# Kernel optimization log

Measured on AMD Instinct MI355X. Metric: run time of the kernel, lower is better.

## Reference

```python
import jax, jax.numpy as jnp
import numpy as np

B, T, D, U = 64, 4096, 256, 64

def setup_inputs() -> dict:
    key = jax.random.key(0)
    k1, k2, k3 = jax.random.split(key, 3)
    inputs = jax.random.normal(k1, (B, T, D), dtype=jnp.float32)
    # glorot_uniform init for W (D,U) and u (U,1); zeros bias
    limW = float(np.sqrt(6.0 / (D + U)))
    W = jax.random.uniform(k2, (D, U), minval=-limW, maxval=limW, dtype=jnp.float32)
    limu = float(np.sqrt(6.0 / (U + 1)))
    u = jax.random.uniform(k3, (U, 1), minval=-limu, maxval=limu, dtype=jnp.float32)
    b = jnp.zeros((U,), dtype=jnp.float32)
    return {"inputs": inputs, "W": W, "b": b, "u": u}

def reference(inputs, W, b, u):
    # score: [B,T,U] = tanh(inputs @ W + b)
    score = jnp.tanh(jnp.einsum('btd,du->btu', inputs, W) + b)
    # logits: [B,T,1]; softmax over time axis (axis=1)
    logits = jnp.einsum('btu,uo->bto', score, u)
    attention_weights = jax.nn.softmax(logits, axis=1)
    # weighted sum over time -> [B,D]
    context = jnp.sum(inputs * attention_weights, axis=1)
    return (context, attention_weights)
```

## Files before the change

kernel.cpp:

```cpp
#include <hip/hip_runtime.h>
#include <math.h>

#define B_ 64
#define T_ 4096
#define D_ 256
#define U_ 64
#define BPB 8
#define RPB (T_ / BPB)
#define NCH (RPB / 64)

typedef float f32x4 __attribute__((ext_vector_type(4)));
typedef short bf16x8 __attribute__((ext_vector_type(8)));

__device__ __forceinline__ unsigned short f2bf_rne(float f) {
    unsigned u = __float_as_uint(f);
    unsigned r = u + 0x7fffu + ((u >> 16) & 1u);
    return (unsigned short)(r >> 16);
}
__device__ __forceinline__ float bfbits2f(unsigned short s) {
    return __uint_as_float(((unsigned)s) << 16);
}

__global__ __launch_bounds__(256) void wprep_kernel(
    const float* __restrict__ W, unsigned short* __restrict__ whi,
    unsigned short* __restrict__ wlo)
{
    int fi = blockIdx.x * 256 + threadIdx.x;
    int j    = fi & 7;
    int lane = (fi >> 3) & 63;
    int tile = fi >> 9;
    int nt = tile & 3, ks = tile >> 2;
    int k = ks * 32 + (lane >> 4) * 8 + j;
    int n = nt * 16 + (lane & 15);
    float w = W[k * U_ + n];
    unsigned short hi = f2bf_rne(w);
    unsigned short lo = f2bf_rne(w - bfbits2f(hi));
    whi[fi] = hi;
    wlo[fi] = lo;
}

__global__ __launch_bounds__(256, 2) void fused_main(
    const float* __restrict__ x, const unsigned short* __restrict__ whi,
    const unsigned short* __restrict__ wlo, const float* __restrict__ bias,
    const float* __restrict__ uvec, float* __restrict__ wts,
    float* __restrict__ Zp, float* __restrict__ Pp)
{
    __shared__ unsigned short Bh[16384];
    __shared__ unsigned short Bl[16384];
    __shared__ float esh[RPB];
    __shared__ float zred[4];

    int tid = threadIdx.x;
    {
        const uint4* sh = (const uint4*)whi;
        const uint4* sl = (const uint4*)wlo;
        uint4* dh = (uint4*)Bh;
        uint4* dl = (uint4*)Bl;
#pragma unroll
        for (int i = 0; i < 8; ++i) {
            dh[tid + i * 256] = sh[tid + i * 256];
            dl[tid + i * 256] = sl[tid + i * 256];
        }
    }
    __syncthreads();

    int lane = tid & 63, wid = tid >> 6;
    int q = lane >> 4, r = lane & 15;
    int b = blockIdx.x / BPB;
    int pb = blockIdx.x % BPB;
    size_t row00 = (size_t)b * T_ + (size_t)pb * RPB;
    const float* xlane = x + (row00 + wid * 16 + r) * D_ + q * 8;
    float* wbase = wts + row00;

    const bf16x8* BhV = (const bf16x8*)Bh;
    const bf16x8* BlV = (const bf16x8*)Bl;

    float zacc = 0.f;

#pragma unroll 1
    for (int c = 0; c < NCH; ++c) {
        const float* xp = xlane + (size_t)c * 64 * D_;
        float4 xb[16];
#pragma unroll
        for (int ks = 0; ks < 8; ++ks) {
            xb[2 * ks]     = *(const float4*)(xp + ks * 32);
            xb[2 * ks + 1] = *(const float4*)(xp + ks * 32 + 4);
        }

        f32x4 acc[4];
#pragma unroll
        for (int nt = 0; nt < 4; ++nt) acc[nt] = (f32x4){0.f, 0.f, 0.f, 0.f};

#pragma unroll
        for (int ks = 0; ks < 8; ++ks) {
            float4 va = xb[2 * ks], vb = xb[2 * ks + 1];
            float f[8] = {va.x, va.y, va.z, va.w, vb.x, vb.y, vb.z, vb.w};
            union { bf16x8 v; unsigned short s[8]; } hi_, lo_;
#pragma unroll
            for (int j = 0; j < 8; ++j) {
                unsigned short a = f2bf_rne(f[j]);
                hi_.s[j] = a;
                lo_.s[j] = f2bf_rne(f[j] - bfbits2f(a));
            }
#pragma unroll
            for (int nt = 0; nt < 4; ++nt) {
                bf16x8 bh = BhV[(ks * 4 + nt) * 64 + lane];
                bf16x8 bl = BlV[(ks * 4 + nt) * 64 + lane];
                acc[nt] = __builtin_amdgcn_mfma_f32_16x16x32_bf16(hi_.v, bh, acc[nt], 0, 0, 0);
                acc[nt] = __builtin_amdgcn_mfma_f32_16x16x32_bf16(hi_.v, bl, acc[nt], 0, 0, 0);
                acc[nt] = __builtin_amdgcn_mfma_f32_16x16x32_bf16(lo_.v, bh, acc[nt], 0, 0, 0);
            }
        }

        float p0 = 0.f, p1 = 0.f, p2 = 0.f, p3 = 0.f;
#pragma unroll
        for (int nt = 0; nt < 4; ++nt) {
            int col = nt * 16 + r;
            float bv = bias[col], uv = uvec[col];
            float s0 = acc[nt][0] + bv, s1 = acc[nt][1] + bv,
                  s2 = acc[nt][2] + bv, s3 = acc[nt][3] + bv;
            p0 = fmaf(1.f - 2.f / (__expf(2.f * s0) + 1.f), uv, p0);
            p1 = fmaf(1.f - 2.f / (__expf(2.f * s1) + 1.f), uv, p1);
            p2 = fmaf(1.f - 2.f / (__expf(2.f * s2) + 1.f), uv, p2);
            p3 = fmaf(1.f - 2.f / (__expf(2.f * s3) + 1.f), uv, p3);
        }
#pragma unroll
        for (int off = 1; off < 16; off <<= 1) {
            p0 += __shfl_xor(p0, off, 64);
            p1 += __shfl_xor(p1, off, 64);
            p2 += __shfl_xor(p2, off, 64);
            p3 += __shfl_xor(p3, off, 64);
        }
        float e0 = __expf(p0), e1 = __expf(p1), e2 = __expf(p2), e3 = __expf(p3);
        if (r == 0) {
            float4 o = {e0, e1, e2, e3};
            int lr = c * 64 + wid * 16 + q * 4;
            *(float4*)(wbase + lr) = o;
            *(float4*)(&esh[lr]) = o;
        }
        zacc += (e0 + e1) + (e2 + e3);
    }

    zacc += __shfl_xor(zacc, 16, 64);
    zacc += __shfl_xor(zacc, 32, 64);
    if (lane == 0) zred[wid] = zacc;
    __syncthreads();
    if (tid == 0) Zp[blockIdx.x] = (zred[0] + zred[1]) + (zred[2] + zred[3]);

    const float* xc = x + row00 * D_ + tid;
    float P0 = 0.f, P1 = 0.f, P2 = 0.f, P3 = 0.f;
#pragma unroll 2
    for (int row = 0; row < RPB; row += 8) {
        float e0 = esh[row + 0], e1 = esh[row + 1], e2 = esh[row + 2], e3 = esh[row + 3];
        float e4 = esh[row + 4], e5 = esh[row + 5], e6 = esh[row + 6], e7 = esh[row + 7];
        float x0 = xc[(size_t)(row + 0) * D_];
        float x1 = xc[(size_t)(row + 1) * D_];
        float x2 = xc[(size_t)(row + 2) * D_];
        float x3 = xc[(size_t)(row + 3) * D_];
        float x4 = xc[(size_t)(row + 4) * D_];
        float x5 = xc[(size_t)(row + 5) * D_];
        float x6 = xc[(size_t)(row + 6) * D_];
        float x7 = xc[(size_t)(row + 7) * D_];
        P0 = fmaf(e0, x0, P0); P1 = fmaf(e1, x1, P1);
        P2 = fmaf(e2, x2, P2); P3 = fmaf(e3, x3, P3);
        P0 = fmaf(e4, x4, P0); P1 = fmaf(e5, x5, P1);
        P2 = fmaf(e6, x6, P2); P3 = fmaf(e7, x7, P3);
    }
    Pp[(size_t)blockIdx.x * D_ + tid] = (P0 + P1) + (P2 + P3);
}

__global__ __launch_bounds__(256) void finalize_kernel(
    float* __restrict__ wts, const float* __restrict__ Zp,
    const float* __restrict__ Pp, float* __restrict__ ctx)
{
    int b = blockIdx.x;
    int tid = threadIdx.x;
    float Z = 0.f;
#pragma unroll
    for (int i = 0; i < BPB; ++i) Z += Zp[b * BPB + i];
    float invZ = 1.f / Z;

    float s = 0.f;
#pragma unroll
    for (int i = 0; i < BPB; ++i) s += Pp[(size_t)(b * BPB + i) * D_ + tid];
    ctx[b * D_ + tid] = s * invZ;

    float4* wp = (float4*)(wts + (size_t)b * T_);
#pragma unroll
    for (int i = 0; i < T_ / 4 / 256; ++i) {
        float4 v = wp[tid + i * 256];
        v.x *= invZ; v.y *= invZ; v.z *= invZ; v.w *= invZ;
        wp[tid + i * 256] = v;
    }
}

extern "C" void kernel_launch(void* const* d_in, const int* in_sizes, int n_in,
                              void* d_out, int out_size, void* d_ws, size_t ws_size,
                              hipStream_t stream) {
    const float* x    = (const float*)d_in[0];
    const float* W    = (const float*)d_in[1];
    const float* bias = (const float*)d_in[2];
    const float* uvec = (const float*)d_in[3];

    float* out = (float*)d_out;
    float* ctx = out;
    float* wts = out + B_ * D_;

    unsigned short* whi = (unsigned short*)d_ws;
    unsigned short* wlo = whi + D_ * U_;
    float* Zp = (float*)(wlo + D_ * U_);
    float* Pp = Zp + B_ * BPB;

    wprep_kernel<<<D_ * U_ / 256, 256, 0, stream>>>(W, whi, wlo);
    fused_main<<<B_ * BPB, 256, 0, stream>>>(x, whi, wlo, bias, uvec, wts, Zp, Pp);
    finalize_kernel<<<B_, 256, 0, stream>>>(wts, Zp, Pp, ctx);
}
```

Before: 454.5 us.

## Split GEMM columns across waves and stage bf16 x in LDS for context

Blocks now cover 64 rows instead of 512, so the grid grows eightfold. Each wave owns one 16-column slice of U and keeps its W hi/lo fragments in registers instead of LDS. The bf16-hi copy of x is stored in LDS, and the weighted-sum pass reads it from there rather than re-reading fp32 x from global memory, removing the second pass over x. The costs are that every wave now reads and splits the same x rows (4x redundant loads and conversion ALU work), context is accumulated from bf16-rounded x, and finalize has more partials to reduce.

```diff
diff --git a/kernel.cpp b/kernel.cpp
--- a/kernel.cpp
+++ b/kernel.cpp
@@ -5,9 +5,10 @@
 #define T_ 4096
 #define D_ 256
 #define U_ 64
-#define BPB 8
-#define RPB (T_ / BPB)
-#define NCH (RPB / 64)
+#define RPB 64
+#define NPB (T_ / RPB)
+#define NSTRIP (RPB / 16)
+#define XPAD 264
 
 typedef float f32x4 __attribute__((ext_vector_type(4)));
 typedef short bf16x8 __attribute__((ext_vector_type(8)));
@@ -39,91 +40,77 @@
     wlo[fi] = lo;
 }
 
-__global__ __launch_bounds__(256, 2) void fused_main(
+__global__ __launch_bounds__(256, 4) void fused_main(
     const float* __restrict__ x, const unsigned short* __restrict__ whi,
     const unsigned short* __restrict__ wlo, const float* __restrict__ bias,
     const float* __restrict__ uvec, float* __restrict__ wts,
     float* __restrict__ Zp, float* __restrict__ Pp)
 {
-    __shared__ unsigned short Bh[16384];
-    __shared__ unsigned short Bl[16384];
+    __shared__ unsigned short Xh[RPB * XPAD];
+    __shared__ float part[RPB][4];
     __shared__ float esh[RPB];
-    __shared__ float zred[4];
 
     int tid = threadIdx.x;
-    {
-        const uint4* sh = (const uint4*)whi;
-        const uint4* sl = (const uint4*)wlo;
-        uint4* dh = (uint4*)Bh;
-        uint4* dl = (uint4*)Bl;
-#pragma unroll
-        for (int i = 0; i < 8; ++i) {
-            dh[tid + i * 256] = sh[tid + i * 256];
-            dl[tid + i * 256] = sl[tid + i * 256];
-        }
-    }
-    __syncthreads();
-
     int lane = tid & 63, wid = tid >> 6;
     int q = lane >> 4, r = lane & 15;
-    int b = blockIdx.x / BPB;
-    int pb = blockIdx.x % BPB;
+
+    bf16x8 Bh[8], Bl[8];
+    {
+        const bf16x8* whiV = (const bf16x8*)whi;
+        const bf16x8* wloV = (const bf16x8*)wlo;
+#pragma unroll
+        for (int ks = 0; ks < 8; ++ks) {
+            Bh[ks] = whiV[(ks * 4 + wid) * 64 + lane];
+            Bl[ks] = wloV[(ks * 4 + wid) * 64 + lane];
+        }
+    }
+
+    int b = blockIdx.x / NPB;
+    int pb = blockIdx.x % NPB;
     size_t row00 = (size_t)b * T_ + (size_t)pb * RPB;
-    const float* xlane = x + (row00 + wid * 16 + r) * D_ + q * 8;
-    float* wbase = wts + row00;
-
-    const bf16x8* BhV = (const bf16x8*)Bh;
-    const bf16x8* BlV = (const bf16x8*)Bl;
-
-    float zacc = 0.f;
+
+    int col = wid * 16 + r;
+    float bv = bias[col], uv = uvec[col];
+
+    const float* xrow = x + (row00 + r) * D_ + q * 8;
 
 #pragma unroll 1
-    for (int c = 0; c < NCH; ++c) {
-        const float* xp = xlane + (size_t)c * 64 * D_;
-        float4 xb[16];
-#pragma unroll
-        for (int ks = 0; ks < 8; ++ks) {
-            xb[2 * ks]     = *(const float4*)(xp + ks * 32);
-            xb[2 * ks + 1] = *(const float4*)(xp + ks * 32 + 4);
-        }
-
-        f32x4 acc[4];
-#pragma unroll
-        for (int nt = 0; nt < 4; ++nt) acc[nt] = (f32x4){0.f, 0.f, 0.f, 0.f};
-
-#pragma unroll
-        for (int ks = 0; ks < 8; ++ks) {
-            float4 va = xb[2 * ks], vb = xb[2 * ks + 1];
-            float f[8] = {va.x, va.y, va.z, va.w, vb.x, vb.y, vb.z, vb.w};
-            union { bf16x8 v; unsigned short s[8]; } hi_, lo_;
-#pragma unroll
-            for (int j = 0; j < 8; ++j) {
-                unsigned short a = f2bf_rne(f[j]);
-                hi_.s[j] = a;
-                lo_.s[j] = f2bf_rne(f[j] - bfbits2f(a));
+    for (int s = 0; s < NSTRIP; ++s) {
+        const float* xp = xrow + (size_t)s * 16 * D_;
+        f32x4 acc = (f32x4){0.f, 0.f, 0.f, 0.f};
+
+#pragma unroll
+        for (int h = 0; h < 2; ++h) {
+            float4 xb[8];
+#pragma unroll
+            for (int k2 = 0; k2 < 4; ++k2) {
+                xb[2 * k2]     = *(const float4*)(xp + (h * 4 + k2) * 32);
+                xb[2 * k2 + 1] = *(const float4*)(xp + (h * 4 + k2) * 32 + 4);
             }
 #pragma unroll
-            for (int nt = 0; nt < 4; ++nt) {
-                bf16x8 bh = BhV[(ks * 4 + nt) * 64 + lane];
-                bf16x8 bl = BlV[(ks * 4 + nt) * 64 + lane];
-                acc[nt] = __builtin_amdgcn_mfma_f32_16x16x32_bf16(hi_.v, bh, acc[nt], 0, 0, 0);
-                acc[nt] = __builtin_amdgcn_mfma_f32_16x16x32_bf16(hi_.v, bl, acc[nt], 0, 0, 0);
-                acc[nt] = __builtin_amdgcn_mfma_f32_16x16x32_bf16(lo_.v, bh, acc[nt], 0, 0, 0);
+            for (int k2 = 0; k2 < 4; ++k2) {
+                int ks = h * 4 + k2;
+                float4 va = xb[2 * k2], vb = xb[2 * k2 + 1];
+                float f[8] = {va.x, va.y, va.z, va.w, vb.x, vb.y, vb.z, vb.w};
+                union { bf16x8 v; unsigned short sh[8]; uint4 u; } hi_, lo_;
+#pragma unroll
+                for (int j = 0; j < 8; ++j) {
+                    unsigned short a = f2bf_rne(f[j]);
+                    hi_.sh[j] = a;
+                    lo_.sh[j] = f2bf_rne(f[j] - bfbits2f(a));
+                }
+                if (wid == 0)
+                    *(uint4*)(&Xh[(s * 16 + r) * XPAD + ks * 32 + q * 8]) = hi_.u;
+                acc = __builtin_amdgcn_mfma_f32_16x16x32_bf16(hi_.v, Bh[ks], acc, 0, 0, 0);
+                acc = __builtin_amdgcn_mfma_f32_16x16x32_bf16(hi_.v, Bl[ks], acc, 0, 0, 0);
+                acc = __builtin_amdgcn_mfma_f32_16x16x32_bf16(lo_.v, Bh[ks], acc, 0, 0, 0);
             }
         }
 
-        float p0 = 0.f, p1 = 0.f, p2 = 0.f, p3 = 0.f;
-#pragma unroll
-        for (int nt = 0; nt < 4; ++nt) {
-            int col = nt * 16 + r;
-            float bv = bias[col], uv = uvec[col];
-            float s0 = acc[nt][0] + bv, s1 = acc[nt][1] + bv,
-                  s2 = acc[nt][2] + bv, s3 = acc[nt][3] + bv;
-            p0 = fmaf(1.f - 2.f / (__expf(2.f * s0) + 1.f), uv, p0);
-            p1 = fmaf(1.f - 2.f / (__expf(2.f * s1) + 1.f), uv, p1);
-            p2 = fmaf(1.f - 2.f / (__expf(2.f * s2) + 1.f), uv, p2);
-            p3 = fmaf(1.f - 2.f / (__expf(2.f * s3) + 1.f), uv, p3);
-        }
+        float p0 = fmaf(1.f - 2.f / (__expf(2.f * (acc[0] + bv)) + 1.f), uv, 0.f);
+        float p1 = fmaf(1.f - 2.f / (__expf(2.f * (acc[1] + bv)) + 1.f), uv, 0.f);
+        float p2 = fmaf(1.f - 2.f / (__expf(2.f * (acc[2] + bv)) + 1.f), uv, 0.f);
+        float p3 = fmaf(1.f - 2.f / (__expf(2.f * (acc[3] + bv)) + 1.f), uv, 0.f);
 #pragma unroll
         for (int off = 1; off < 16; off <<= 1) {
             p0 += __shfl_xor(p0, off, 64);
@@ -131,42 +118,51 @@
             p2 += __shfl_xor(p2, off, 64);
             p3 += __shfl_xor(p3, off, 64);
         }
-        float e0 = __expf(p0), e1 = __expf(p1), e2 = __expf(p2), e3 = __expf(p3);
         if (r == 0) {
-            float4 o = {e0, e1, e2, e3};
-            int lr = c * 64 + wid * 16 + q * 4;
-            *(float4*)(wbase + lr) = o;
-            *(float4*)(&esh[lr]) = o;
-        }
-        zacc += (e0 + e1) + (e2 + e3);
-    }
-
-    zacc += __shfl_xor(zacc, 16, 64);
-    zacc += __shfl_xor(zacc, 32, 64);
-    if (lane == 0) zred[wid] = zacc;
-    __syncthreads();
-    if (tid == 0) Zp[blockIdx.x] = (zred[0] + zred[1]) + (zred[2] + zred[3]);
-
-    const float* xc = x + row00 * D_ + tid;
-    float P0 = 0.f, P1 = 0.f, P2 = 0.f, P3 = 0.f;
+            int row = s * 16 + q * 4;
+            part[row + 0][wid] = p0;
+            part[row + 1][wid] = p1;
+            part[row + 2][wid] = p2;
+            part[row + 3][wid] = p3;
+        }
+    }
+    __syncthreads();
+
+    if (wid == 0) {
+        float lg = (part[lane][0] + part[lane][1]) + (part[lane][2] + part[lane][3]);
+        float e = __expf(lg);
+        esh[lane] = e;
+        wts[row00 + lane] = e;
+        float z = e;
+#pragma unroll
+        for (int off = 1; off < 64; off <<= 1) z += __shfl_xor(z, off, 64);
+        if (lane == 0) Zp[blockIdx.x] = z;
+    }
+    __syncthreads();
+
+    int colg = tid & 31, ph = tid >> 5;
+    float pacc[8];
+#pragma unroll
+    for (int j = 0; j < 8; ++j) pacc[j] = 0.f;
 #pragma unroll 2
-    for (int row = 0; row < RPB; row += 8) {
-        float e0 = esh[row + 0], e1 = esh[row + 1], e2 = esh[row + 2], e3 = esh[row + 3];
-        float e4 = esh[row + 4], e5 = esh[row + 5], e6 = esh[row + 6], e7 = esh[row + 7];
-        float x0 = xc[(size_t)(row + 0) * D_];
-        float x1 = xc[(size_t)(row + 1) * D_];
-        float x2 = xc[(size_t)(row + 2) * D_];
-        float x3 = xc[(size_t)(row + 3) * D_];
-        float x4 = xc[(size_t)(row + 4) * D_];
-        float x5 = xc[(size_t)(row + 5) * D_];
-        float x6 = xc[(size_t)(row + 6) * D_];
-        float x7 = xc[(size_t)(row + 7) * D_];
-        P0 = fmaf(e0, x0, P0); P1 = fmaf(e1, x1, P1);
-        P2 = fmaf(e2, x2, P2); P3 = fmaf(e3, x3, P3);
-        P0 = fmaf(e4, x4, P0); P1 = fmaf(e5, x5, P1);
-        P2 = fmaf(e6, x6, P2); P3 = fmaf(e7, x7, P3);
-    }
-    Pp[(size_t)blockIdx.x * D_ + tid] = (P0 + P1) + (P2 + P3);
+    for (int i = 0; i < RPB; i += 8) {
+        int row = i + ph;
+        float w = esh[row];
+        union { uint4 u; unsigned short sh[8]; } v;
+        v.u = *(const uint4*)(&Xh[row * XPAD + colg * 8]);
+#pragma unroll
+        for (int j = 0; j < 8; ++j)
+            pacc[j] = fmaf(w, bfbits2f(v.sh[j]), pacc[j]);
+    }
+    __syncthreads();
+    float* red = (float*)Xh;
+#pragma unroll
+    for (int j = 0; j < 8; ++j) red[ph * 256 + colg * 8 + j] = pacc[j];
+    __syncthreads();
+    float ssum = 0.f;
+#pragma unroll
+    for (int p = 0; p < 8; ++p) ssum += red[p * 256 + tid];
+    Pp[(size_t)blockIdx.x * D_ + tid] = ssum;
 }
 
 __global__ __launch_bounds__(256) void finalize_kernel(
@@ -176,13 +172,13 @@
     int b = blockIdx.x;
     int tid = threadIdx.x;
     float Z = 0.f;
-#pragma unroll
-    for (int i = 0; i < BPB; ++i) Z += Zp[b * BPB + i];
+#pragma unroll 8
+    for (int i = 0; i < NPB; ++i) Z += Zp[b * NPB + i];
     float invZ = 1.f / Z;
 
     float s = 0.f;
-#pragma unroll
-    for (int i = 0; i < BPB; ++i) s += Pp[(size_t)(b * BPB + i) * D_ + tid];
+#pragma unroll 4
+    for (int i = 0; i < NPB; ++i) s += Pp[(size_t)(b * NPB + i) * D_ + tid];
     ctx[b * D_ + tid] = s * invZ;
 
     float4* wp = (float4*)(wts + (size_t)b * T_);
@@ -209,9 +205,9 @@
     unsigned short* whi = (unsigned short*)d_ws;
     unsigned short* wlo = whi + D_ * U_;
     float* Zp = (float*)(wlo + D_ * U_);
-    float* Pp = Zp + B_ * BPB;
+    float* Pp = Zp + B_ * NPB;
 
     wprep_kernel<<<D_ * U_ / 256, 256, 0, stream>>>(W, whi, wlo);
-    fused_main<<<B_ * BPB, 256, 0, stream>>>(x, whi, wlo, bias, uvec, wts, Zp, Pp);
+    fused_main<<<(B_ * T_) / RPB, 256, 0, stream>>>(x, whi, wlo, bias, uvec, wts, Zp, Pp);
     finalize_kernel<<<B_, 256, 0, stream>>>(wts, Zp, Pp, ctx);
 }
```

After: 411.0 us. 9.6% less time.
